# Performance work log

Measured on AMD Instinct MI355X. Metric: run time of the kernel, lower is better.

Reference implementation:

```python
import jax, jax.numpy as jnp
import numpy as np

CLIP_MIN = 0.0  # recurrent_clip_min resolved in build() when -1
CLIP_MAX = 1.0  # recurrent_clip_max default when timesteps unknown


def setup_inputs() -> dict:
    key = jax.random.key(0)
    k1, k2, k3 = jax.random.split(key, 3)
    B, T, D, U = 64, 512, 256, 512
    x = jax.random.normal(k1, (B, T, D), dtype=jnp.float32)
    h0 = jnp.zeros((B, U), dtype=jnp.float32)
    W = jax.random.normal(k2, (D, U), dtype=jnp.float32) * (1.0 / np.sqrt(D))
    u = jax.random.uniform(k3, (U,), dtype=jnp.float32)  # uniform in clip range
    b = jnp.zeros((U,), dtype=jnp.float32)
    return {"x": x, "h0": h0, "W": W, "u": u, "b": b}


def reference(x, h0, W, u, b):
    # IndRNN: h_t = relu(x_t @ W + h_{t-1} * u + b), u clipped to [0, 1]
    u_c = jnp.clip(u, CLIP_MIN, CLIP_MAX)
    # One-time input projection for all timesteps: [B,T,U]
    proj = jnp.einsum("btd,du->btu", x, W) + b
    proj_t = jnp.swapaxes(proj, 0, 1)  # [T,B,U] for scan over time

    def step(h, p_t):
        h_new = jax.nn.relu(p_t + h * u_c)
        return h_new, h_new

    _, hs = jax.lax.scan(step, h0, proj_t)  # hs: [T,B,U]
    return jnp.swapaxes(hs, 0, 1)  # [B,T,U]
```

## Files before the change

kernel.cpp:

```cpp
#include <hip/hip_runtime.h>


__device__ __forceinline__ unsigned short f2bf(float f) {
    unsigned int u = __float_as_uint(f);
    unsigned int r = (u + 0x7FFF + ((u >> 16) & 1)) >> 16;
    return (unsigned short)r;
}

typedef __bf16 bf16x8 __attribute__((ext_vector_type(8)));
typedef float f32x4 __attribute__((ext_vector_type(4)));

typedef const unsigned char __attribute__((address_space(1))) gc_t;
typedef unsigned char __attribute__((address_space(3))) lds_t;

__device__ __forceinline__ void gl_lds16(const void* g, void* l) {
    __builtin_amdgcn_global_load_lds((gc_t*)g, (lds_t*)l, 16, 0, 0);
}

__global__ __launch_bounds__(256) void conv_xw(
    const float* __restrict__ x, unsigned short* __restrict__ xb, int nx4,
    const float* __restrict__ W, unsigned short* __restrict__ Wt, int K, int N)
{
    int i = blockIdx.x * blockDim.x + threadIdx.x;
    if (i < nx4) {
        float4 v = *(const float4*)(x + (long)i * 4);
        ushort4 o;
        o.x = f2bf(v.x); o.y = f2bf(v.y); o.z = f2bf(v.z); o.w = f2bf(v.w);
        *(ushort4*)(xb + (long)i * 4) = o;
        return;
    }
    int idx = i - nx4;
    int kq = K >> 2;
    if (idx >= N * kq) return;
    int n = idx / kq;
    int k4 = (idx - n * kq) * 4;
    ushort4 o;
    o.x = f2bf(W[(long)(k4 + 0) * N + n]);
    o.y = f2bf(W[(long)(k4 + 1) * N + n]);
    o.z = f2bf(W[(long)(k4 + 2) * N + n]);
    o.w = f2bf(W[(long)(k4 + 3) * N + n]);
    *(ushort4*)(Wt + (long)n * K + k4) = o;
}

#define TC 64
#define GN 64

__global__ __launch_bounds__(256, 2) void indrnn_fused(
    const unsigned short* __restrict__ xb,
    const unsigned short* __restrict__ wt,
    const float* __restrict__ bias,
    const float* __restrict__ h0,
    const float* __restrict__ uvec,
    float* __restrict__ out,
    int B, int T, int U)
{
    __shared__ __align__(16) char  Xa[2][TC * 512];
    __shared__ __align__(16) float P[TC * GN];

    const int tid  = threadIdx.x;
    const int lane = tid & 63;
    const int w    = tid >> 6;
    const int m    = lane & 15;
    const int quad = lane >> 4;
    const int b    = blockIdx.x;
    const int n0   = blockIdx.y * GN;
    const int tq   = w * 16;

    bf16x8 bfr[4][8];
#pragma unroll
    for (int j = 0; j < 4; ++j)
#pragma unroll
        for (int kt = 0; kt < 8; ++kt)
            bfr[j][kt] = *(const bf16x8*)(
                wt + (long)(n0 + j * 16 + m) * 256 + kt * 32 + quad * 8);

    float bb[4];
#pragma unroll
    for (int j = 0; j < 4; ++j) bb[j] = bias[n0 + j * 16 + m];

    float uc = 0.0f, h = 0.0f;
    if (tid < GN) {
        uc = fminf(fmaxf(uvec[n0 + tid], 0.0f), 1.0f);
        h  = h0[(long)b * U + n0 + tid];
    }

    const unsigned short* xrow = xb + (long)b * T * 256;

    {
        const int p = lane & 31, hh = lane >> 5;
#pragma unroll
        for (int i = 0; i < 8; ++i) {
            int blk = i * 4 + w;
            int r   = 2 * blk + hh;
            int gp  = p ^ (r & 15);
            gl_lds16(xrow + (long)r * 256 + gp * 8, &Xa[0][blk * 1024]);
        }
    }

    const int nch = T / TC;
    for (int c = 0; c < nch; ++c) {
        const char* Xc = Xa[c & 1];
        __syncthreads();

        f32x4 acc[4];
#pragma unroll
        for (int j = 0; j < 4; ++j) acc[j] = (f32x4){0.f, 0.f, 0.f, 0.f};

#pragma unroll
        for (int kt = 0; kt < 8; ++kt) {
            bf16x8 a = *(const bf16x8*)(
                Xc + (tq + m) * 512 + (((kt * 4 + quad) ^ m) << 4));
#pragma unroll
            for (int j = 0; j < 4; ++j)
                acc[j] = __builtin_amdgcn_mfma_f32_16x16x32_bf16(
                    a, bfr[j][kt], acc[j], 0, 0, 0);
        }

#pragma unroll
        for (int j = 0; j < 4; ++j)
#pragma unroll
            for (int r = 0; r < 4; ++r) {
                int tl = tq + quad * 4 + r;
                int cs = (j * 16 + m) ^ (quad << 4);
                P[tl * GN + cs] = acc[j][r] + bb[j];
            }
        __syncthreads();

        if (w >= 2) {
            if (c + 1 < nch) {
                const unsigned short* gb = xrow + (long)(c + 1) * TC * 256;
                char* Xn = Xa[(c + 1) & 1];
                const int p = lane & 31, hh = lane >> 5;
#pragma unroll
                for (int i = 0; i < 16; ++i) {
                    int blk = i * 2 + (w - 2);
                    int r   = 2 * blk + hh;
                    int gp  = p ^ (r & 15);
                    gl_lds16(gb + (long)r * 256 + gp * 8, Xn + blk * 1024);
                }
            }
        } else if (w == 0) {
            float* og = out + ((long)b * T + (long)c * TC) * U + n0 + lane;
#pragma unroll 16
            for (int t = 0; t < TC; ++t) {
                float pv = P[t * GN + (lane ^ (((t >> 2) & 3) << 4))];
                h = fmaxf(fmaf(h, uc, pv), 0.0f);
                og[(long)t * U] = h;
            }
        }
    }
}

#define BM 128
#define BN 128
#define BK 8

__global__ __launch_bounds__(256) void indrnn_gemm_bias(
    const float* __restrict__ A, const float* __restrict__ Bm,
    const float* __restrict__ bias, float* __restrict__ C,
    int M, int N, int K)
{
    __shared__ float As[BK][BM];
    __shared__ float Bs[BK][BN];
    const int tid = threadIdx.x;
    const int row0 = blockIdx.x * BM, col0 = blockIdx.y * BN;
    const int tx = tid & 15, ty = tid >> 4;
    float acc[8][8];
#pragma unroll
    for (int i = 0; i < 8; ++i)
#pragma unroll
        for (int j = 0; j < 8; ++j) acc[i][j] = 0.0f;
    const int am = tid >> 1, ak = (tid & 1) * 4;
    const int bk = tid >> 5, bn = (tid & 31) * 4;
    const float* Aptr = A + (long)(row0 + am) * K + ak;
    const float* Bptr = Bm + (long)bk * N + col0 + bn;
    for (int kt = 0; kt < K; kt += BK) {
        float4 av = *(const float4*)(Aptr + kt);
        float4 bv = *(const float4*)(Bptr + (long)kt * N);
        As[ak + 0][am] = av.x; As[ak + 1][am] = av.y;
        As[ak + 2][am] = av.z; As[ak + 3][am] = av.w;
        *(float4*)&Bs[bk][bn] = bv;
        __syncthreads();
#pragma unroll
        for (int k = 0; k < BK; ++k) {
            float4 a0 = *(const float4*)&As[k][ty * 4];
            float4 a1 = *(const float4*)&As[k][64 + ty * 4];
            float4 b0 = *(const float4*)&Bs[k][tx * 4];
            float4 b1 = *(const float4*)&Bs[k][64 + tx * 4];
            float a[8] = {a0.x, a0.y, a0.z, a0.w, a1.x, a1.y, a1.z, a1.w};
            float bb2[8] = {b0.x, b0.y, b0.z, b0.w, b1.x, b1.y, b1.z, b1.w};
#pragma unroll
            for (int i = 0; i < 8; ++i)
#pragma unroll
                for (int j = 0; j < 8; ++j)
                    acc[i][j] = fmaf(a[i], bb2[j], acc[i][j]);
        }
        __syncthreads();
    }
    float bb[8];
#pragma unroll
    for (int j = 0; j < 4; ++j) {
        bb[j] = bias[col0 + tx * 4 + j];
        bb[j + 4] = bias[col0 + 64 + tx * 4 + j];
    }
#pragma unroll
    for (int i = 0; i < 8; ++i) {
        const int r = (i < 4) ? (ty * 4 + i) : (64 + ty * 4 + (i - 4));
        float* crow = C + (long)(row0 + r) * N + col0;
        float4 v0 = {acc[i][0] + bb[0], acc[i][1] + bb[1], acc[i][2] + bb[2], acc[i][3] + bb[3]};
        float4 v1 = {acc[i][4] + bb[4], acc[i][5] + bb[5], acc[i][6] + bb[6], acc[i][7] + bb[7]};
        *(float4*)(crow + tx * 4) = v0;
        *(float4*)(crow + 64 + tx * 4) = v1;
    }
}

#define SCAN_UNROLL 32

__global__ __launch_bounds__(256) void indrnn_scan(
    float* __restrict__ out, const float* __restrict__ h0,
    const float* __restrict__ u, int B, int T, int U)
{
    const int idx = blockIdx.x * blockDim.x + threadIdx.x;
    if (idx >= B * U) return;
    const int b = idx / U;
    const int un = idx - b * U;
    const float uc = fminf(fmaxf(u[un], 0.0f), 1.0f);
    float h = h0[(long)b * U + un];
    float* p = out + (long)b * T * U + un;
    for (int t = 0; t < T; t += SCAN_UNROLL) {
        float pv[SCAN_UNROLL];
#pragma unroll
        for (int i = 0; i < SCAN_UNROLL; ++i)
            pv[i] = p[(long)(t + i) * U];
#pragma unroll
        for (int i = 0; i < SCAN_UNROLL; ++i) {
            h = fmaxf(fmaf(h, uc, pv[i]), 0.0f);
            pv[i] = h;
        }
#pragma unroll
        for (int i = 0; i < SCAN_UNROLL; ++i)
            p[(long)(t + i) * U] = pv[i];
    }
}

extern "C" void kernel_launch(void* const* d_in, const int* in_sizes, int n_in,
                              void* d_out, int out_size, void* d_ws, size_t ws_size,
                              hipStream_t stream) {
    const float* x  = (const float*)d_in[0];
    const float* h0 = (const float*)d_in[1];
    const float* W  = (const float*)d_in[2];
    const float* u  = (const float*)d_in[3];
    const float* b  = (const float*)d_in[4];
    float* out = (float*)d_out;

    const int U = in_sizes[3];
    const int B = in_sizes[1] / U;
    const int D = in_sizes[2] / U;
    const int T = in_sizes[0] / (B * D);
    const int M = B * T;

    const size_t xb_bytes = (size_t)M * D * sizeof(unsigned short);
    const size_t wt_bytes = (size_t)U * D * sizeof(unsigned short);
    const bool fused_ok = (D == 256) && (U % GN == 0) && (T % TC == 0) &&
                          (ws_size >= xb_bytes + wt_bytes);

    if (fused_ok) {
        unsigned short* xb = (unsigned short*)d_ws;
        unsigned short* wt = (unsigned short*)((char*)d_ws + xb_bytes);

        const int nx4 = (M * D) / 4;
        const int nwt = U * (D / 4);
        const int ntot = nx4 + nwt;
        conv_xw<<<(ntot + 255) / 256, 256, 0, stream>>>(x, xb, nx4, W, wt, D, U);

        dim3 g(B, U / GN);
        indrnn_fused<<<g, 256, 0, stream>>>(xb, wt, b, h0, u, out, B, T, U);
    } else {
        dim3 ggrid(M / BM, U / BN);
        indrnn_gemm_bias<<<ggrid, 256, 0, stream>>>(x, W, b, out, M, U, D);
        const int nthreads = B * U;
        indrnn_scan<<<(nthreads + 255) / 256, 256, 0, stream>>>(out, h0, u, B, T, U);
    }
}
```

Baseline: 127.8 us.

## Fuse bf16 conversion into IndRNN kernel and drop separate conversion pass

Removes the separate conv_xw kernel that wrote bf16 copies of x and a transposed W to workspace. The fused kernel now streams fp32 x straight into LDS and converts to bf16 at fragment-load time, and builds the W fragments from fp32 with strided loads. This saves a full read/write pass over x and one kernel launch. The chunk shrinks to 32 timesteps so the fp32 tiles fit in LDS, and two waves run the MFMAs while two prefetch, which changes the balance between compute, loads and the serial scan.

New measurement: 220.9 us. 1.73x slower.

```diff
diff --git a/kernel.cpp b/kernel.cpp
--- a/kernel.cpp
+++ b/kernel.cpp
@@ -1,11 +1,6 @@
 #include <hip/hip_runtime.h>
-
-
-__device__ __forceinline__ unsigned short f2bf(float f) {
-    unsigned int u = __float_as_uint(f);
-    unsigned int r = (u + 0x7FFF + ((u >> 16) & 1)) >> 16;
-    return (unsigned short)r;
-}
+#include <hip/hip_bf16.h>
+
 
 typedef __bf16 bf16x8 __attribute__((ext_vector_type(8)));
 typedef float f32x4 __attribute__((ext_vector_type(4)));
@@ -17,44 +12,21 @@
     __builtin_amdgcn_global_load_lds((gc_t*)g, (lds_t*)l, 16, 0, 0);
 }
 
-__global__ __launch_bounds__(256) void conv_xw(
-    const float* __restrict__ x, unsigned short* __restrict__ xb, int nx4,
-    const float* __restrict__ W, unsigned short* __restrict__ Wt, int K, int N)
-{
-    int i = blockIdx.x * blockDim.x + threadIdx.x;
-    if (i < nx4) {
-        float4 v = *(const float4*)(x + (long)i * 4);
-        ushort4 o;
-        o.x = f2bf(v.x); o.y = f2bf(v.y); o.z = f2bf(v.z); o.w = f2bf(v.w);
-        *(ushort4*)(xb + (long)i * 4) = o;
-        return;
-    }
-    int idx = i - nx4;
-    int kq = K >> 2;
-    if (idx >= N * kq) return;
-    int n = idx / kq;
-    int k4 = (idx - n * kq) * 4;
-    ushort4 o;
-    o.x = f2bf(W[(long)(k4 + 0) * N + n]);
-    o.y = f2bf(W[(long)(k4 + 1) * N + n]);
-    o.z = f2bf(W[(long)(k4 + 2) * N + n]);
-    o.w = f2bf(W[(long)(k4 + 3) * N + n]);
-    *(ushort4*)(Wt + (long)n * K + k4) = o;
-}
-
-#define TC 64
+union bfu { bf16x8 v; __hip_bfloat162 h[4]; };
+
+#define TC 32
 #define GN 64
 
 __global__ __launch_bounds__(256, 2) void indrnn_fused(
-    const unsigned short* __restrict__ xb,
-    const unsigned short* __restrict__ wt,
+    const float* __restrict__ x,
+    const float* __restrict__ W,
     const float* __restrict__ bias,
     const float* __restrict__ h0,
     const float* __restrict__ uvec,
     float* __restrict__ out,
     int B, int T, int U)
 {
-    __shared__ __align__(16) char  Xa[2][TC * 512];
+    __shared__ __align__(16) float Xa[2][TC * 256];
     __shared__ __align__(16) float P[TC * GN];
 
     const int tid  = threadIdx.x;
@@ -64,15 +36,25 @@
     const int quad = lane >> 4;
     const int b    = blockIdx.x;
     const int n0   = blockIdx.y * GN;
-    const int tq   = w * 16;
-
-    bf16x8 bfr[4][8];
-#pragma unroll
-    for (int j = 0; j < 4; ++j)
-#pragma unroll
-        for (int kt = 0; kt < 8; ++kt)
-            bfr[j][kt] = *(const bf16x8*)(
-                wt + (long)(n0 + j * 16 + m) * 256 + kt * 32 + quad * 8);
+    const int tq   = (w & 1) * 16;
+
+    bfu bfr[4][8];
+    if (w < 2) {
+#pragma unroll
+        for (int j = 0; j < 4; ++j)
+#pragma unroll
+            for (int kt = 0; kt < 8; ++kt) {
+                const float* wp =
+                    W + (long)(kt * 32 + quad * 8) * U + n0 + j * 16 + m;
+                float f[8];
+#pragma unroll
+                for (int e = 0; e < 8; ++e) f[e] = wp[(long)e * U];
+                bfr[j][kt].h[0] = __float22bfloat162_rn(make_float2(f[0], f[1]));
+                bfr[j][kt].h[1] = __float22bfloat162_rn(make_float2(f[2], f[3]));
+                bfr[j][kt].h[2] = __float22bfloat162_rn(make_float2(f[4], f[5]));
+                bfr[j][kt].h[3] = __float22bfloat162_rn(make_float2(f[6], f[7]));
+            }
+    }
 
     float bb[4];
 #pragma unroll
@@ -84,64 +66,65 @@
         h  = h0[(long)b * U + n0 + tid];
     }
 
-    const unsigned short* xrow = xb + (long)b * T * 256;
-
-    {
-        const int p = lane & 31, hh = lane >> 5;
-#pragma unroll
-        for (int i = 0; i < 8; ++i) {
-            int blk = i * 4 + w;
-            int r   = 2 * blk + hh;
-            int gp  = p ^ (r & 15);
-            gl_lds16(xrow + (long)r * 256 + gp * 8, &Xa[0][blk * 1024]);
-        }
+    const float* xg = x + (long)b * T * 256;
+
+#pragma unroll
+    for (int i = 0; i < 8; ++i) {
+        int r = w + i * 4;
+        gl_lds16(xg + (long)r * 256 + ((lane ^ (r & 15)) << 2),
+                 (char*)Xa[0] + r * 1024);
     }
 
     const int nch = T / TC;
     for (int c = 0; c < nch; ++c) {
-        const char* Xc = Xa[c & 1];
-        __syncthreads();
-
-        f32x4 acc[4];
-#pragma unroll
-        for (int j = 0; j < 4; ++j) acc[j] = (f32x4){0.f, 0.f, 0.f, 0.f};
-
-#pragma unroll
-        for (int kt = 0; kt < 8; ++kt) {
-            bf16x8 a = *(const bf16x8*)(
-                Xc + (tq + m) * 512 + (((kt * 4 + quad) ^ m) << 4));
-#pragma unroll
-            for (int j = 0; j < 4; ++j)
-                acc[j] = __builtin_amdgcn_mfma_f32_16x16x32_bf16(
-                    a, bfr[j][kt], acc[j], 0, 0, 0);
-        }
-
-#pragma unroll
-        for (int j = 0; j < 4; ++j)
-#pragma unroll
-            for (int r = 0; r < 4; ++r) {
-                int tl = tq + quad * 4 + r;
-                int cs = (j * 16 + m) ^ (quad << 4);
-                P[tl * GN + cs] = acc[j][r] + bb[j];
-            }
+        const f32x4* XF = (const f32x4*)Xa[c & 1];
         __syncthreads();
 
         if (w >= 2) {
             if (c + 1 < nch) {
-                const unsigned short* gb = xrow + (long)(c + 1) * TC * 256;
-                char* Xn = Xa[(c + 1) & 1];
-                const int p = lane & 31, hh = lane >> 5;
+                const float* gn = xg + (long)(c + 1) * TC * 256;
+                float* Xn = Xa[(c + 1) & 1];
 #pragma unroll
                 for (int i = 0; i < 16; ++i) {
-                    int blk = i * 2 + (w - 2);
-                    int r   = 2 * blk + hh;
-                    int gp  = p ^ (r & 15);
-                    gl_lds16(gb + (long)r * 256 + gp * 8, Xn + blk * 1024);
+                    int r = (w - 2) + i * 2;
+                    gl_lds16(gn + (long)r * 256 + ((lane ^ (r & 15)) << 2),
+                             (char*)Xn + r * 1024);
                 }
             }
-        } else if (w == 0) {
+        } else {
+            f32x4 acc[4];
+#pragma unroll
+            for (int j = 0; j < 4; ++j) acc[j] = (f32x4){0.f, 0.f, 0.f, 0.f};
+
+#pragma unroll
+            for (int kt = 0; kt < 8; ++kt) {
+                const int c0 = kt * 8 + quad * 2;
+                const int rowb = (tq + m) * 64;
+                f32x4 p0 = XF[rowb + (c0 ^ m)];
+                f32x4 p1 = XF[rowb + ((c0 + 1) ^ m)];
+                bfu a;
+                a.h[0] = __float22bfloat162_rn(make_float2(p0.x, p0.y));
+                a.h[1] = __float22bfloat162_rn(make_float2(p0.z, p0.w));
+                a.h[2] = __float22bfloat162_rn(make_float2(p1.x, p1.y));
+                a.h[3] = __float22bfloat162_rn(make_float2(p1.z, p1.w));
+#pragma unroll
+                for (int j = 0; j < 4; ++j)
+                    acc[j] = __builtin_amdgcn_mfma_f32_16x16x32_bf16(
+                        a.v, bfr[j][kt].v, acc[j], 0, 0, 0);
+            }
+
+#pragma unroll
+            for (int j = 0; j < 4; ++j)
+#pragma unroll
+                for (int r = 0; r < 4; ++r)
+                    P[(tq + quad * 4 + r) * GN + ((j * 16 + m) ^ (quad << 4))] =
+                        acc[j][r] + bb[j];
+        }
+        __syncthreads();
+
+        if (w == 0) {
             float* og = out + ((long)b * T + (long)c * TC) * U + n0 + lane;
-#pragma unroll 16
+#pragma unroll
             for (int t = 0; t < TC; ++t) {
                 float pv = P[t * GN + (lane ^ (((t >> 2) & 3) << 4))];
                 h = fmaxf(fmaf(h, uc, pv), 0.0f);
@@ -259,22 +242,11 @@
     const int T = in_sizes[0] / (B * D);
     const int M = B * T;
 
-    const size_t xb_bytes = (size_t)M * D * sizeof(unsigned short);
-    const size_t wt_bytes = (size_t)U * D * sizeof(unsigned short);
-    const bool fused_ok = (D == 256) && (U % GN == 0) && (T % TC == 0) &&
-                          (ws_size >= xb_bytes + wt_bytes);
+    const bool fused_ok = (D == 256) && (U % GN == 0) && (T % TC == 0);
 
     if (fused_ok) {
-        unsigned short* xb = (unsigned short*)d_ws;
-        unsigned short* wt = (unsigned short*)((char*)d_ws + xb_bytes);
-
-        const int nx4 = (M * D) / 4;
-        const int nwt = U * (D / 4);
-        const int ntot = nx4 + nwt;
-        conv_xw<<<(ntot + 255) / 256, 256, 0, stream>>>(x, xb, nx4, W, wt, D, U);
-
         dim3 g(B, U / GN);
-        indrnn_fused<<<g, 256, 0, stream>>>(xb, wt, b, h0, u, out, B, T, U);
+        indrnn_fused<<<g, 256, 0, stream>>>(x, W, b, h0, u, out, B, T, U);
     } else {
         dim3 ggrid(M / BM, U / BN);
         indrnn_gemm_bias<<<ggrid, 256, 0, stream>>>(x, W, b, out, M, U, D);
```
